# Kernel optimization log

Hardware: AMD Instinct MI355X
Metric: run time of the kernel (lower is better)

Reference implementation:

```python
import jax, jax.numpy as jnp
import numpy as np

BETA = 0.9
GAMMA = -0.1
EPSILON = 2.0
LAMBDA = 1e-4

B, COLS, FEAT, E = 16384, 32, 500000, 16
ACC = COLS * E          # 512
NE = 8                  # num_experts
SBH = 256               # SB_hidden
SBO = 128               # SB_output
TH = 16                 # towers_hidden
T = 2                   # num_tasks


def setup_inputs() -> dict:
    key = jax.random.key(0)
    ks = jax.random.split(key, 16)
    eps = 1e-4
    return {
        "x": jax.random.randint(ks[0], (B, COLS), 0, FEAT, dtype=jnp.int64 if jax.config.jax_enable_x64 else jnp.int32),
        "emb": jax.random.normal(ks[1], (FEAT, E), dtype=jnp.float32),
        "alpha1": jax.random.uniform(ks[2], (1,), minval=eps, maxval=1.0, dtype=jnp.float32),
        "u1": jax.random.uniform(ks[3], (ACC, NE, SBH), minval=eps, maxval=1.0 - eps, dtype=jnp.float32),
        "w1": jax.random.normal(ks[4], (ACC, NE, SBH), dtype=jnp.float32) * np.sqrt(2.0 / (ACC + SBH)),
        "alpha2": jax.random.uniform(ks[5], (1,), minval=eps, maxval=1.0, dtype=jnp.float32),
        "u2": jax.random.uniform(ks[6], (SBH, SBO), minval=eps, maxval=1.0 - eps, dtype=jnp.float32),
        "w2": jax.random.normal(ks[7], (SBH, SBO), dtype=jnp.float32) * np.sqrt(2.0 / (SBH + SBO)),
        "fce_w": jax.random.normal(ks[8], (1, NE), dtype=jnp.float32) * 0.1,
        "fce_b": jnp.zeros((1,), dtype=jnp.float32),
        "tw1": jax.random.normal(ks[9], (T, SBO, TH), dtype=jnp.float32) * np.sqrt(1.0 / SBO),
        "tb1": jnp.zeros((T, TH), dtype=jnp.float32),
        "tw2": jax.random.normal(ks[10], (T, TH, 1), dtype=jnp.float32) * np.sqrt(1.0 / TH),
        "tb2": jnp.zeros((T, 1), dtype=jnp.float32),
    }


def _hard_concrete(u, alpha):
    # s = sigmoid(log u - log(1-u) + log(alpha)/beta); s_ = s*(eps-gamma)+gamma
    s = jax.nn.sigmoid(jnp.log(u) - jnp.log(1.0 - u) + jnp.log(alpha) / BETA)
    s_ = s * (EPSILON - GAMMA) + GAMMA
    # z = (s_>0)*s_ then clamp above at 1  == clip(s_, 0, 1)
    z = jnp.clip(s_, 0.0, 1.0)
    return s_, z


def reference(x, emb, alpha1, u1, w1, alpha2, u2, w2, fce_w, fce_b, tw1, tb1, tw2, tb2):
    # embedding gather + field concat -> [B, COLS*E]
    xf = emb[x].reshape(x.shape[0], -1)
    s1_, z1 = _hard_concrete(u1, alpha1)
    o = jnp.einsum('ab,bnc->anc', xf, z1 * w1)          # [B, NE, SBH]
    s2_, z2 = _hard_concrete(u2, alpha2)
    o = jnp.einsum('anc,cd->and', o, z2 * w2)           # [B, NE, SBO]
    o = jnp.swapaxes(o, 1, 2)                           # [B, SBO, NE]
    o = o @ fce_w.T + fce_b                             # [B, SBO, 1]
    o = jax.nn.relu(jnp.squeeze(o, -1))                 # [B, SBO]
    # per-task towers (dropout is inference no-op)
    h = jax.nn.relu(jnp.einsum('bd,tdh->tbh', o, tw1) + tb1[:, None, :])
    outs = jax.nn.sigmoid(jnp.einsum('tbh,tho->tbo', h, tw2) + tb2[:, None, :])  # [T, B, 1]
    # L0-style regularizer (integer ops, zero gradient)
    s1_prob = 1 - (s1_ < 0).sum(axis=-1) // s1_.shape[1]
    s2_prob = 1 - (s2_ < 0).sum(axis=-1) // s2_.shape[1]
    regul = LAMBDA * (s1_prob.sum() + s2_prob.sum()).astype(jnp.float32)
    return outs, regul
```

## Files before the change

kernel.cpp:

```cpp
#include <hip/hip_runtime.h>
#include <hip/hip_bf16.h>
#include <math.h>

#define B_ROWS 16384
#define NCOLS 32
#define EDIM 16
#define ACCD 512
#define NE 8
#define SBH 256
#define SBO 128
#define THD 16
#define NT 2

#define ROWS 32
#define THR 512

typedef __attribute__((ext_vector_type(8))) short bf16x8;
typedef __attribute__((ext_vector_type(4))) float f32x4;
typedef __attribute__((ext_vector_type(16))) float f32x16;

__device__ __forceinline__ short f2bf(float f) {
    unsigned u = __float_as_uint(f);
    unsigned r = (u + 0x7FFFu + ((u >> 16) & 1u)) >> 16;
    return (short)r;
}

__device__ __forceinline__ bf16x8 pack8(float4 a, float4 b) {
    bf16x8 v;
    v[0] = f2bf(a.x); v[1] = f2bf(a.y); v[2] = f2bf(a.z); v[3] = f2bf(a.w);
    v[4] = f2bf(b.x); v[5] = f2bf(b.y); v[6] = f2bf(b.z); v[7] = f2bf(b.w);
    return v;
}


__global__ __launch_bounds__(256) void k_prep(const float* __restrict__ u1,
                                              const float* __restrict__ w1,
                                              const float* __restrict__ alpha1,
                                              const float* __restrict__ fce_w,
                                              const float* __restrict__ u2,
                                              const float* __restrict__ w2,
                                              const float* __restrict__ alpha2,
                                              const float* __restrict__ tw1,
                                              short* __restrict__ W1cF,
                                              short* __restrict__ W2F,
                                              short* __restrict__ tw1T,
                                              int* __restrict__ regparts) {
    const int bid = blockIdx.x;
    const int tid = threadIdx.x;
    if (bid < 512) {
        const int a = bid, c = tid;
        const float A = expf(-logf(alpha1[0]) * (1.0f / 0.9f));
        __shared__ int cnts[NE];
        if (c < NE) cnts[c] = 0;
        __syncthreads();
        float acc = 0.0f;
        #pragma unroll
        for (int n = 0; n < NE; ++n) {
            const int idx = (a * NE + n) * SBH + c;
            const float u = u1[idx];
            const float s = u / (u + (1.0f - u) * A);
            const float s_ = s * 2.1f - 0.1f;
            const float z = fminf(fmaxf(s_, 0.0f), 1.0f);
            acc += z * w1[idx] * fce_w[n];
            unsigned long long m = __ballot(s_ < 0.0f);
            if ((c & 63) == 0) atomicAdd(&cnts[n], __popcll(m));
        }
        __syncthreads();
        {
            const int ks = a >> 4, kr = a & 15;
            const int sub = kr >> 3, j = kr & 7;
            const int cg = c >> 5, lane = (sub << 5) | (c & 31);
            W1cF[(((ks * 8 + cg) * 64) + lane) * 8 + j] = f2bf(acc);
        }
        if (c == 0) {
            int tot = 0;
            #pragma unroll
            for (int n = 0; n < NE; ++n) tot += 1 - cnts[n] / NE;
            regparts[a] = tot;
        }
    } else if (bid < 640) {
        const int c = (bid - 512) * 2 + (tid >> 7);
        const int d = tid & 127;
        const float A = expf(-logf(alpha2[0]) * (1.0f / 0.9f));
        const int idx = c * SBO + d;
        const float u = u2[idx];
        const float s = u / (u + (1.0f - u) * A);
        const float s_ = s * 2.1f - 0.1f;
        const float z = fminf(fmaxf(s_, 0.0f), 1.0f);
        {
            const int ks = c >> 5, krem = c & 31;
            const int sub = krem >> 3, j = krem & 7;
            const int cg = d >> 4, lane = (sub << 4) | (d & 15);
            W2F[(((ks * 8 + cg) * 64) + lane) * 8 + j] = f2bf(z * w2[idx]);
        }
        __shared__ int cnts2[2];
        if (tid < 2) cnts2[tid] = 0;
        __syncthreads();
        unsigned long long m = __ballot(s_ < 0.0f);
        if ((tid & 63) == 0) atomicAdd(&cnts2[tid >> 7], __popcll(m));
        __syncthreads();
        if ((tid & 127) == 0) regparts[ACCD + c] = 1 - cnts2[tid >> 7] / SBO;
    } else {
        #pragma unroll
        for (int i = 0; i < 16; ++i) {
            const int e = tid * 16 + i;
            const int jj = e >> 7;
            const int d = e & 127;
            tw1T[jj * SBO + d] = f2bf(tw1[((jj >> 4) * SBO + d) * THD + (jj & 15)]);
        }
    }
}

#define MFMA32(a, b, c) __builtin_amdgcn_mfma_f32_32x32x16_bf16((a), (b), (c), 0, 0, 0)
#define MFMA16(a, b, c) __builtin_amdgcn_mfma_f32_16x16x32_bf16((a), (b), (c), 0, 0, 0)

#define LDS_T 32768
#define LDS_O 49152

__global__ __launch_bounds__(THR, 4) void k_main(const int* __restrict__ x,
                                                 const float* __restrict__ emb,
                                                 const short* __restrict__ W1cF,
                                                 const short* __restrict__ W2F,
                                                 const short* __restrict__ tw1T,
                                                 const float* __restrict__ fce_b,
                                                 const float* __restrict__ tb1,
                                                 const float* __restrict__ tw2,
                                                 const float* __restrict__ tb2,
                                                 const int* __restrict__ regparts,
                                                 float* __restrict__ outp) {
    __shared__ __align__(16) char lds[57344];

    const int tid = threadIdx.x;
    const int l = tid & 63;
    const int w = tid >> 6;
    const int lrow32 = l & 31;
    const int hg = l >> 5;
    const int lrow16 = l & 15;
    const int lg4 = (l >> 4) & 3;
    const int rowbase = blockIdx.x * ROWS;

    const int srow = tid >> 4;
    const int scol = tid & 15;
    char* sbase = lds + (srow << 10);
    const int sswz = (srow & 15) << 4;

    const int xv0 = x[(rowbase + srow) * NCOLS + scol];
    const int xv1 = x[(rowbase + srow) * NCOLS + 16 + scol];

    {
        const float4* ep = reinterpret_cast<const float4*>(emb + (size_t)xv0 * EDIM);
        const float4 e0 = ep[0], e1 = ep[1], e2 = ep[2], e3 = ep[3];
        *(bf16x8*)(sbase + ((scol * 32 + 0) ^ sswz))  = pack8(e0, e1);
        *(bf16x8*)(sbase + ((scol * 32 + 16) ^ sswz)) = pack8(e2, e3);
    }
    const float4* ep1 = reinterpret_cast<const float4*>(emb + (size_t)xv1 * EDIM);
    const float4 g0 = ep1[0], g1 = ep1[1], g2 = ep1[2], g3 = ep1[3];
    __syncthreads();

    char* aAb = lds + (lrow32 << 10);
    const int aswz = (lrow32 & 15) << 4;
    const bf16x8* Bp = ((const bf16x8*)W1cF) + l;

    f32x16 acc;
    #pragma unroll
    for (int i = 0; i < 16; ++i) acc[i] = 0.0f;

    bf16x8 b0 = Bp[(0 * 8 + w) * 64];
    bf16x8 b1 = Bp[(1 * 8 + w) * 64];
    bf16x8 b2 = Bp[(2 * 8 + w) * 64];
    bf16x8 b3 = Bp[(3 * 8 + w) * 64];

    #pragma unroll
    for (int ks = 0; ks < 16; ks += 4) {
        { const bf16x8 a = *(const bf16x8*)(aAb + ((((ks + 0) * 32) + hg * 16) ^ aswz));
          acc = MFMA32(a, b0, acc); b0 = Bp[((ks + 4) * 8 + w) * 64]; }
        { const bf16x8 a = *(const bf16x8*)(aAb + ((((ks + 1) * 32) + hg * 16) ^ aswz));
          acc = MFMA32(a, b1, acc); b1 = Bp[((ks + 5) * 8 + w) * 64]; }
        { const bf16x8 a = *(const bf16x8*)(aAb + ((((ks + 2) * 32) + hg * 16) ^ aswz));
          acc = MFMA32(a, b2, acc); b2 = Bp[((ks + 6) * 8 + w) * 64]; }
        { const bf16x8 a = *(const bf16x8*)(aAb + ((((ks + 3) * 32) + hg * 16) ^ aswz));
          acc = MFMA32(a, b3, acc); b3 = Bp[((ks + 7) * 8 + w) * 64]; }
    }
    *(bf16x8*)(sbase + (((16 + scol) * 32 + 0) ^ sswz))  = pack8(g0, g1);
    *(bf16x8*)(sbase + (((16 + scol) * 32 + 16) ^ sswz)) = pack8(g2, g3);
    __syncthreads();

    #pragma unroll
    for (int ks = 16; ks < 32; ks += 4) {
        { const bf16x8 a = *(const bf16x8*)(aAb + ((((ks + 0) * 32) + hg * 16) ^ aswz));
          acc = MFMA32(a, b0, acc); if (ks + 4 < 32) b0 = Bp[((ks + 4) * 8 + w) * 64]; }
        { const bf16x8 a = *(const bf16x8*)(aAb + ((((ks + 1) * 32) + hg * 16) ^ aswz));
          acc = MFMA32(a, b1, acc); if (ks + 5 < 32) b1 = Bp[((ks + 5) * 8 + w) * 64]; }
        { const bf16x8 a = *(const bf16x8*)(aAb + ((((ks + 2) * 32) + hg * 16) ^ aswz));
          acc = MFMA32(a, b2, acc); if (ks + 6 < 32) b2 = Bp[((ks + 6) * 8 + w) * 64]; }
        { const bf16x8 a = *(const bf16x8*)(aAb + ((((ks + 3) * 32) + hg * 16) ^ aswz));
          acc = MFMA32(a, b3, acc); if (ks + 7 < 32) b3 = Bp[((ks + 7) * 8 + w) * 64]; }
    }

    const int cgA = (w & 3) * 2;
    const int rg2 = w >> 2;
    const bf16x8* Bp2 = ((const bf16x8*)W2F) + l;
    bf16x8 q0a = Bp2[(0 * 8 + cgA) * 64], q0b = Bp2[(0 * 8 + cgA + 1) * 64];
    bf16x8 q1a = Bp2[(1 * 8 + cgA) * 64], q1b = Bp2[(1 * 8 + cgA + 1) * 64];

    {
        const int tcol2 = (w * 32 + lrow32) * 2;
        #pragma unroll
        for (int r = 0; r < 16; ++r) {
            const int trow = (r & 3) + 8 * (r >> 2) + 4 * hg;
            *(short*)(lds + LDS_T + (trow << 9) + (tcol2 ^ ((trow & 15) << 4))) = f2bf(acc[r]);
        }
    }
    __syncthreads();

    f32x4 acc2[2];
    acc2[0] = (f32x4){0.f, 0.f, 0.f, 0.f};
    acc2[1] = (f32x4){0.f, 0.f, 0.f, 0.f};
    {
        char* tAb = lds + LDS_T + ((rg2 * 16 + lrow16) << 9);
        const int tswz = (lrow16 & 15) << 4;
        #pragma unroll
        for (int kc = 0; kc < 8; kc += 2) {
            { const bf16x8 a = *(const bf16x8*)(tAb + ((((kc + 0) * 64) + lg4 * 16) ^ tswz));
              acc2[0] = MFMA16(a, q0a, acc2[0]);
              acc2[1] = MFMA16(a, q0b, acc2[1]);
              if (kc + 2 < 8) { q0a = Bp2[((kc + 2) * 8 + cgA) * 64]; q0b = Bp2[((kc + 2) * 8 + cgA + 1) * 64]; } }
            { const bf16x8 a = *(const bf16x8*)(tAb + ((((kc + 1) * 64) + lg4 * 16) ^ tswz));
              acc2[0] = MFMA16(a, q1a, acc2[0]);
              acc2[1] = MFMA16(a, q1b, acc2[1]);
              if (kc + 3 < 8) { q1a = Bp2[((kc + 3) * 8 + cgA) * 64]; q1b = Bp2[((kc + 3) * 8 + cgA + 1) * 64]; } }
        }
    }

    {
        const float fb = fce_b[0];
        #pragma unroll
        for (int fd = 0; fd < 2; ++fd) {
            const int d2 = ((cgA + fd) * 16 + lrow16) * 2;
            #pragma unroll
            for (int rr = 0; rr < 4; ++rr) {
                const int orow = rg2 * 16 + lg4 * 4 + rr;
                *(short*)(lds + LDS_O + (orow << 8) + (d2 ^ ((orow & 15) << 4))) =
                    f2bf(fmaxf(acc2[fd][rr] + fb, 0.0f));
            }
        }
    }
    __syncthreads();

    if (w < 4) {
        const int rtt = w >> 1, ct = w & 1;
        f32x4 h = (f32x4){0.f, 0.f, 0.f, 0.f};
        char* oAb = lds + LDS_O + ((rtt * 16 + lrow16) << 8);
        const int oswz = (lrow16 & 15) << 4;
        const short* bT = tw1T + (ct * 16 + lrow16) * SBO + lg4 * 8;
        #pragma unroll
        for (int kc = 0; kc < 4; ++kc) {
            const bf16x8 av = *(const bf16x8*)(oAb + ((kc * 64 + lg4 * 16) ^ oswz));
            const bf16x8 bv = *(const bf16x8*)(bT + kc * 32);
            h = MFMA16(av, bv, h);
        }
        const float b1v = tb1[ct * THD + lrow16];
        const float w2v = tw2[ct * THD + lrow16];
        float p[4];
        #pragma unroll
        for (int rr = 0; rr < 4; ++rr) {
            p[rr] = fmaxf(h[rr] + b1v, 0.0f) * w2v;
            #pragma unroll
            for (int off = 8; off >= 1; off >>= 1)
                p[rr] += __shfl_xor(p[rr], off);
        }
        if (lrow16 == 0) {
            const float b2v = tb2[ct];
            #pragma unroll
            for (int rr = 0; rr < 4; ++rr) {
                const int rowo = rtt * 16 + lg4 * 4 + rr;
                outp[ct * B_ROWS + rowbase + rowo] = 1.0f / (1.0f + __expf(-(p[rr] + b2v)));
            }
        }
    }

    if (blockIdx.x == 0 && tid < 64) {
        int s = 0;
        for (int i = tid; i < ACCD + SBH; i += 64) s += regparts[i];
        #pragma unroll
        for (int off = 32; off > 0; off >>= 1) s += __shfl_down(s, off);
        if (tid == 0) outp[NT * B_ROWS] = 1e-4f * (float)s;
    }
}

extern "C" void kernel_launch(void* const* d_in, const int* in_sizes, int n_in,
                              void* d_out, int out_size, void* d_ws, size_t ws_size,
                              hipStream_t stream) {
    const int*   x      = (const int*)d_in[0];
    const float* emb    = (const float*)d_in[1];
    const float* alpha1 = (const float*)d_in[2];
    const float* u1     = (const float*)d_in[3];
    const float* w1     = (const float*)d_in[4];
    const float* alpha2 = (const float*)d_in[5];
    const float* u2     = (const float*)d_in[6];
    const float* w2     = (const float*)d_in[7];
    const float* fce_w  = (const float*)d_in[8];
    const float* fce_b  = (const float*)d_in[9];
    const float* tw1    = (const float*)d_in[10];
    const float* tb1    = (const float*)d_in[11];
    const float* tw2    = (const float*)d_in[12];
    const float* tb2    = (const float*)d_in[13];
    float* outp = (float*)d_out;

    short* W1cF = (short*)d_ws;
    short* W2F  = W1cF + 32 * 8 * 64 * 8;
    short* tw1T = W2F + 8 * 8 * 64 * 8;
    int*   regparts = (int*)(tw1T + NT * THD * SBO);

    k_prep<<<641, 256, 0, stream>>>(u1, w1, alpha1, fce_w, u2, w2, alpha2, tw1,
                                    W1cF, W2F, tw1T, regparts);
    k_main<<<B_ROWS / ROWS, THR, 0, stream>>>(x, emb, W1cF, W2F, tw1T, fce_b,
                                              tb1, tw2, tb2, regparts, outp);
}
```

Measured before the change: 123.0 us.

## Pre-convert full embedding table to bf16 and gather bf16 rows in main kernel

Adds blocks to the prep kernel that convert the entire fp32 embedding table to a bf16 copy in the workspace. The main kernel then gathers 32-byte bf16 rows instead of 64-byte fp32 rows and loads both halves up front, dropping the split gather/MFMA phase. The output staging buffer now reuses the A-tile LDS region, shrinking LDS so the occupancy hint can rise from 4 to 6. In exchange, every call streams the whole table (about 32MB read, 16MB written), far more data than the roughly 0.5M rows actually gathered.

```diff
diff --git a/kernel.cpp b/kernel.cpp
--- a/kernel.cpp
+++ b/kernel.cpp
@@ -33,6 +33,9 @@
 }
 
 
+#define CONV_BLOCKS 977
+#define CONV_GROUPS 1000000
+
 __global__ __launch_bounds__(256) void k_prep(const float* __restrict__ u1,
                                               const float* __restrict__ w1,
                                               const float* __restrict__ alpha1,
@@ -41,10 +44,12 @@
                                               const float* __restrict__ w2,
                                               const float* __restrict__ alpha2,
                                               const float* __restrict__ tw1,
+                                              const float* __restrict__ emb,
                                               short* __restrict__ W1cF,
                                               short* __restrict__ W2F,
                                               short* __restrict__ tw1T,
-                                              int* __restrict__ regparts) {
+                                              int* __restrict__ regparts,
+                                              short* __restrict__ embB) {
     const int bid = blockIdx.x;
     const int tid = threadIdx.x;
     if (bid < 512) {
@@ -100,7 +105,7 @@
         if ((tid & 63) == 0) atomicAdd(&cnts2[tid >> 7], __popcll(m));
         __syncthreads();
         if ((tid & 127) == 0) regparts[ACCD + c] = 1 - cnts2[tid >> 7] / SBO;
-    } else {
+    } else if (bid == 640) {
         #pragma unroll
         for (int i = 0; i < 16; ++i) {
             const int e = tid * 16 + i;
@@ -108,6 +113,17 @@
             const int d = e & 127;
             tw1T[jj * SBO + d] = f2bf(tw1[((jj >> 4) * SBO + d) * THD + (jj & 15)]);
         }
+    } else {
+        const int base = (bid - 641) * 256 + tid;
+        #pragma unroll
+        for (int i = 0; i < 4; ++i) {
+            const int g = base + i * (CONV_BLOCKS * 256);
+            if (g < CONV_GROUPS) {
+                const float4* sp = reinterpret_cast<const float4*>(emb + (size_t)g * 8);
+                const float4 a = sp[0], b = sp[1];
+                *reinterpret_cast<bf16x8*>(embB + (size_t)g * 8) = pack8(a, b);
+            }
+        }
     }
 }
 
@@ -115,10 +131,9 @@
 #define MFMA16(a, b, c) __builtin_amdgcn_mfma_f32_16x16x32_bf16((a), (b), (c), 0, 0, 0)
 
 #define LDS_T 32768
-#define LDS_O 49152
-
-__global__ __launch_bounds__(THR, 4) void k_main(const int* __restrict__ x,
-                                                 const float* __restrict__ emb,
+
+__global__ __launch_bounds__(THR, 6) void k_main(const int* __restrict__ x,
+                                                 const short* __restrict__ embB,
                                                  const short* __restrict__ W1cF,
                                                  const short* __restrict__ W2F,
                                                  const short* __restrict__ tw1T,
@@ -128,7 +143,7 @@
                                                  const float* __restrict__ tb2,
                                                  const int* __restrict__ regparts,
                                                  float* __restrict__ outp) {
-    __shared__ __align__(16) char lds[57344];
+    __shared__ __align__(16) char lds[49152];
 
     const int tid = threadIdx.x;
     const int l = tid & 63;
@@ -139,22 +154,22 @@
     const int lg4 = (l >> 4) & 3;
     const int rowbase = blockIdx.x * ROWS;
 
-    const int srow = tid >> 4;
-    const int scol = tid & 15;
-    char* sbase = lds + (srow << 10);
-    const int sswz = (srow & 15) << 4;
-
-    const int xv0 = x[(rowbase + srow) * NCOLS + scol];
-    const int xv1 = x[(rowbase + srow) * NCOLS + 16 + scol];
-
     {
-        const float4* ep = reinterpret_cast<const float4*>(emb + (size_t)xv0 * EDIM);
-        const float4 e0 = ep[0], e1 = ep[1], e2 = ep[2], e3 = ep[3];
-        *(bf16x8*)(sbase + ((scol * 32 + 0) ^ sswz))  = pack8(e0, e1);
-        *(bf16x8*)(sbase + ((scol * 32 + 16) ^ sswz)) = pack8(e2, e3);
-    }
-    const float4* ep1 = reinterpret_cast<const float4*>(emb + (size_t)xv1 * EDIM);
-    const float4 g0 = ep1[0], g1 = ep1[1], g2 = ep1[2], g3 = ep1[3];
+        const int srow = tid >> 4;
+        const int scol = tid & 15;
+        char* sbase = lds + (srow << 10);
+        const int sswz = (srow & 15) << 4;
+        const int xv0 = x[(rowbase + srow) * NCOLS + scol];
+        const int xv1 = x[(rowbase + srow) * NCOLS + 16 + scol];
+        const bf16x8* r0 = reinterpret_cast<const bf16x8*>(embB + (size_t)xv0 * EDIM);
+        const bf16x8* r1 = reinterpret_cast<const bf16x8*>(embB + (size_t)xv1 * EDIM);
+        const bf16x8 v00 = r0[0], v01 = r0[1];
+        const bf16x8 v10 = r1[0], v11 = r1[1];
+        *(bf16x8*)(sbase + ((scol * 32 + 0) ^ sswz))  = v00;
+        *(bf16x8*)(sbase + ((scol * 32 + 16) ^ sswz)) = v01;
+        *(bf16x8*)(sbase + (((16 + scol) * 32 + 0) ^ sswz))  = v10;
+        *(bf16x8*)(sbase + (((16 + scol) * 32 + 16) ^ sswz)) = v11;
+    }
     __syncthreads();
 
     char* aAb = lds + (lrow32 << 10);
@@ -171,22 +186,7 @@
     bf16x8 b3 = Bp[(3 * 8 + w) * 64];
 
     #pragma unroll
-    for (int ks = 0; ks < 16; ks += 4) {
-        { const bf16x8 a = *(const bf16x8*)(aAb + ((((ks + 0) * 32) + hg * 16) ^ aswz));
-          acc = MFMA32(a, b0, acc); b0 = Bp[((ks + 4) * 8 + w) * 64]; }
-        { const bf16x8 a = *(const bf16x8*)(aAb + ((((ks + 1) * 32) + hg * 16) ^ aswz));
-          acc = MFMA32(a, b1, acc); b1 = Bp[((ks + 5) * 8 + w) * 64]; }
-        { const bf16x8 a = *(const bf16x8*)(aAb + ((((ks + 2) * 32) + hg * 16) ^ aswz));
-          acc = MFMA32(a, b2, acc); b2 = Bp[((ks + 6) * 8 + w) * 64]; }
-        { const bf16x8 a = *(const bf16x8*)(aAb + ((((ks + 3) * 32) + hg * 16) ^ aswz));
-          acc = MFMA32(a, b3, acc); b3 = Bp[((ks + 7) * 8 + w) * 64]; }
-    }
-    *(bf16x8*)(sbase + (((16 + scol) * 32 + 0) ^ sswz))  = pack8(g0, g1);
-    *(bf16x8*)(sbase + (((16 + scol) * 32 + 16) ^ sswz)) = pack8(g2, g3);
-    __syncthreads();
-
-    #pragma unroll
-    for (int ks = 16; ks < 32; ks += 4) {
+    for (int ks = 0; ks < 32; ks += 4) {
         { const bf16x8 a = *(const bf16x8*)(aAb + ((((ks + 0) * 32) + hg * 16) ^ aswz));
           acc = MFMA32(a, b0, acc); if (ks + 4 < 32) b0 = Bp[((ks + 4) * 8 + w) * 64]; }
         { const bf16x8 a = *(const bf16x8*)(aAb + ((((ks + 1) * 32) + hg * 16) ^ aswz));
@@ -240,7 +240,7 @@
             #pragma unroll
             for (int rr = 0; rr < 4; ++rr) {
                 const int orow = rg2 * 16 + lg4 * 4 + rr;
-                *(short*)(lds + LDS_O + (orow << 8) + (d2 ^ ((orow & 15) << 4))) =
+                *(short*)(lds + (orow << 8) + (d2 ^ ((orow & 15) << 4))) =
                     f2bf(fmaxf(acc2[fd][rr] + fb, 0.0f));
             }
         }
@@ -250,7 +250,7 @@
     if (w < 4) {
         const int rtt = w >> 1, ct = w & 1;
         f32x4 h = (f32x4){0.f, 0.f, 0.f, 0.f};
-        char* oAb = lds + LDS_O + ((rtt * 16 + lrow16) << 8);
+        char* oAb = lds + ((rtt * 16 + lrow16) << 8);
         const int oswz = (lrow16 & 15) << 4;
         const short* bT = tw1T + (ct * 16 + lrow16) * SBO + lg4 * 8;
         #pragma unroll
@@ -311,9 +311,11 @@
     short* W2F  = W1cF + 32 * 8 * 64 * 8;
     short* tw1T = W2F + 8 * 8 * 64 * 8;
     int*   regparts = (int*)(tw1T + NT * THD * SBO);
-
-    k_prep<<<641, 256, 0, stream>>>(u1, w1, alpha1, fce_w, u2, w2, alpha2, tw1,
-                                    W1cF, W2F, tw1T, regparts);
-    k_main<<<B_ROWS / ROWS, THR, 0, stream>>>(x, emb, W1cF, W2F, tw1T, fce_b,
+    short* embB = (short*)(regparts + 768);
+
+    k_prep<<<641 + CONV_BLOCKS, 256, 0, stream>>>(u1, w1, alpha1, fce_w, u2, w2,
+                                                  alpha2, tw1, emb,
+                                                  W1cF, W2F, tw1T, regparts, embB);
+    k_main<<<B_ROWS / ROWS, THR, 0, stream>>>(x, embB, W1cF, W2F, tw1T, fce_b,
                                               tb1, tw2, tb2, regparts, outp);
 }
```

New measurement: 127.4 us. 1.04x slower.

## Prefetch embedding table via sweep blocks in prep kernel and shrink LDS

Applied to the files above, without the earlier changes.

Adds 512 extra blocks to the prep kernel that stream-read the whole embedding table, so the random row gathers in the main kernel hit warm cache instead of DRAM. The main kernel now loads both halves of the gathered embeddings up front instead of overlapping the second half with the first MFMAs. It also reuses the A-tile LDS region for the output tile, cutting LDS per block so more blocks may fit on a CU. The trade-off is an extra full sequential pass over the table every call and less overlap between gather and compute.

```diff
diff --git a/kernel.cpp b/kernel.cpp
--- a/kernel.cpp
+++ b/kernel.cpp
@@ -33,6 +33,9 @@
 }
 
 
+#define SWEEP_BLOCKS 512
+#define SWEEP_F4 2000000
+
 __global__ __launch_bounds__(256) void k_prep(const float* __restrict__ u1,
                                               const float* __restrict__ w1,
                                               const float* __restrict__ alpha1,
@@ -41,6 +44,7 @@
                                               const float* __restrict__ w2,
                                               const float* __restrict__ alpha2,
                                               const float* __restrict__ tw1,
+                                              const float* __restrict__ emb,
                                               short* __restrict__ W1cF,
                                               short* __restrict__ W2F,
                                               short* __restrict__ tw1T,
@@ -100,7 +104,7 @@
         if ((tid & 63) == 0) atomicAdd(&cnts2[tid >> 7], __popcll(m));
         __syncthreads();
         if ((tid & 127) == 0) regparts[ACCD + c] = 1 - cnts2[tid >> 7] / SBO;
-    } else {
+    } else if (bid == 640) {
         #pragma unroll
         for (int i = 0; i < 16; ++i) {
             const int e = tid * 16 + i;
@@ -108,6 +112,18 @@
             const int d = e & 127;
             tw1T[jj * SBO + d] = f2bf(tw1[((jj >> 4) * SBO + d) * THD + (jj & 15)]);
         }
+    } else {
+        const int idx = (bid - 641) * 256 + tid;
+        float accw = 0.0f;
+        #pragma unroll
+        for (int i = 0; i < 16; ++i) {
+            const int g = idx + i * (SWEEP_BLOCKS * 256);
+            if (g < SWEEP_F4) {
+                const float4 v = reinterpret_cast<const float4*>(emb)[g];
+                accw += v.x + v.y + v.z + v.w;
+            }
+        }
+        asm volatile("" :: "v"(accw));
     }
 }
 
@@ -115,7 +131,6 @@
 #define MFMA16(a, b, c) __builtin_amdgcn_mfma_f32_16x16x32_bf16((a), (b), (c), 0, 0, 0)
 
 #define LDS_T 32768
-#define LDS_O 49152
 
 __global__ __launch_bounds__(THR, 4) void k_main(const int* __restrict__ x,
                                                  const float* __restrict__ emb,
@@ -128,7 +143,7 @@
                                                  const float* __restrict__ tb2,
                                                  const int* __restrict__ regparts,
                                                  float* __restrict__ outp) {
-    __shared__ __align__(16) char lds[57344];
+    __shared__ __align__(16) char lds[49152];
 
     const int tid = threadIdx.x;
     const int l = tid & 63;
@@ -139,22 +154,22 @@
     const int lg4 = (l >> 4) & 3;
     const int rowbase = blockIdx.x * ROWS;
 
-    const int srow = tid >> 4;
-    const int scol = tid & 15;
-    char* sbase = lds + (srow << 10);
-    const int sswz = (srow & 15) << 4;
-
-    const int xv0 = x[(rowbase + srow) * NCOLS + scol];
-    const int xv1 = x[(rowbase + srow) * NCOLS + 16 + scol];
-
     {
-        const float4* ep = reinterpret_cast<const float4*>(emb + (size_t)xv0 * EDIM);
-        const float4 e0 = ep[0], e1 = ep[1], e2 = ep[2], e3 = ep[3];
+        const int srow = tid >> 4;
+        const int scol = tid & 15;
+        char* sbase = lds + (srow << 10);
+        const int sswz = (srow & 15) << 4;
+        const int xv0 = x[(rowbase + srow) * NCOLS + scol];
+        const int xv1 = x[(rowbase + srow) * NCOLS + 16 + scol];
+        const float4* r0 = reinterpret_cast<const float4*>(emb + (size_t)xv0 * EDIM);
+        const float4* r1 = reinterpret_cast<const float4*>(emb + (size_t)xv1 * EDIM);
+        const float4 e0 = r0[0], e1 = r0[1], e2 = r0[2], e3 = r0[3];
+        const float4 f0 = r1[0], f1 = r1[1], f2 = r1[2], f3 = r1[3];
         *(bf16x8*)(sbase + ((scol * 32 + 0) ^ sswz))  = pack8(e0, e1);
         *(bf16x8*)(sbase + ((scol * 32 + 16) ^ sswz)) = pack8(e2, e3);
-    }
-    const float4* ep1 = reinterpret_cast<const float4*>(emb + (size_t)xv1 * EDIM);
-    const float4 g0 = ep1[0], g1 = ep1[1], g2 = ep1[2], g3 = ep1[3];
+        *(bf16x8*)(sbase + (((16 + scol) * 32 + 0) ^ sswz))  = pack8(f0, f1);
+        *(bf16x8*)(sbase + (((16 + scol) * 32 + 16) ^ sswz)) = pack8(f2, f3);
+    }
     __syncthreads();
 
     char* aAb = lds + (lrow32 << 10);
@@ -171,22 +186,7 @@
     bf16x8 b3 = Bp[(3 * 8 + w) * 64];
 
     #pragma unroll
-    for (int ks = 0; ks < 16; ks += 4) {
-        { const bf16x8 a = *(const bf16x8*)(aAb + ((((ks + 0) * 32) + hg * 16) ^ aswz));
-          acc = MFMA32(a, b0, acc); b0 = Bp[((ks + 4) * 8 + w) * 64]; }
-        { const bf16x8 a = *(const bf16x8*)(aAb + ((((ks + 1) * 32) + hg * 16) ^ aswz));
-          acc = MFMA32(a, b1, acc); b1 = Bp[((ks + 5) * 8 + w) * 64]; }
-        { const bf16x8 a = *(const bf16x8*)(aAb + ((((ks + 2) * 32) + hg * 16) ^ aswz));
-          acc = MFMA32(a, b2, acc); b2 = Bp[((ks + 6) * 8 + w) * 64]; }
-        { const bf16x8 a = *(const bf16x8*)(aAb + ((((ks + 3) * 32) + hg * 16) ^ aswz));
-          acc = MFMA32(a, b3, acc); b3 = Bp[((ks + 7) * 8 + w) * 64]; }
-    }
-    *(bf16x8*)(sbase + (((16 + scol) * 32 + 0) ^ sswz))  = pack8(g0, g1);
-    *(bf16x8*)(sbase + (((16 + scol) * 32 + 16) ^ sswz)) = pack8(g2, g3);
-    __syncthreads();
-
-    #pragma unroll
-    for (int ks = 16; ks < 32; ks += 4) {
+    for (int ks = 0; ks < 32; ks += 4) {
         { const bf16x8 a = *(const bf16x8*)(aAb + ((((ks + 0) * 32) + hg * 16) ^ aswz));
           acc = MFMA32(a, b0, acc); if (ks + 4 < 32) b0 = Bp[((ks + 4) * 8 + w) * 64]; }
         { const bf16x8 a = *(const bf16x8*)(aAb + ((((ks + 1) * 32) + hg * 16) ^ aswz));
@@ -240,7 +240,7 @@
             #pragma unroll
             for (int rr = 0; rr < 4; ++rr) {
                 const int orow = rg2 * 16 + lg4 * 4 + rr;
-                *(short*)(lds + LDS_O + (orow << 8) + (d2 ^ ((orow & 15) << 4))) =
+                *(short*)(lds + (orow << 8) + (d2 ^ ((orow & 15) << 4))) =
                     f2bf(fmaxf(acc2[fd][rr] + fb, 0.0f));
             }
         }
@@ -250,7 +250,7 @@
     if (w < 4) {
         const int rtt = w >> 1, ct = w & 1;
         f32x4 h = (f32x4){0.f, 0.f, 0.f, 0.f};
-        char* oAb = lds + LDS_O + ((rtt * 16 + lrow16) << 8);
+        char* oAb = lds + ((rtt * 16 + lrow16) << 8);
         const int oswz = (lrow16 & 15) << 4;
         const short* bT = tw1T + (ct * 16 + lrow16) * SBO + lg4 * 8;
         #pragma unroll
@@ -312,8 +312,9 @@
     short* tw1T = W2F + 8 * 8 * 64 * 8;
     int*   regparts = (int*)(tw1T + NT * THD * SBO);
 
-    k_prep<<<641, 256, 0, stream>>>(u1, w1, alpha1, fce_w, u2, w2, alpha2, tw1,
-                                    W1cF, W2F, tw1T, regparts);
+    k_prep<<<641 + SWEEP_BLOCKS, 256, 0, stream>>>(u1, w1, alpha1, fce_w, u2, w2,
+                                                   alpha2, tw1, emb,
+                                                   W1cF, W2F, tw1T, regparts);
     k_main<<<B_ROWS / ROWS, THR, 0, stream>>>(x, emb, W1cF, W2F, tw1T, fce_b,
                                               tb1, tw2, tb2, regparts, outp);
 }
```

Result: slower. 126.5 us (+2.8%).
